# Performance work log

Measured on AMD Instinct MI355X. Metric: run time of the kernel, lower is better.

The kernel has to match this reference:

```python
import jax, jax.numpy as jnp
import numpy as np

N_NODES = 50000
N_EDGES = 400000
NUM_FEATS = 128
LATENT_DIM_Y = 64
HIDDEN = 512
OUT = 2


def gcn_conv(x, edge_index, W, b, num_nodes):
    """PyG GCNConv: add self-loops, symmetric normalization, x @ W then scatter-add."""
    x = x @ W  # [N, out_ch]
    loop = jnp.arange(num_nodes)
    row = jnp.concatenate([edge_index[0], loop])  # source nodes
    col = jnp.concatenate([edge_index[1], loop])  # target nodes
    deg = jax.ops.segment_sum(jnp.ones_like(col, dtype=x.dtype), col, num_segments=num_nodes)
    dinv = jnp.where(deg > 0, jax.lax.rsqrt(deg), 0.0)
    norm = dinv[row] * dinv[col]  # [E+N]
    msgs = norm[:, None] * x[row]  # gather source features, scale
    out = jax.ops.segment_sum(msgs, col, num_segments=num_nodes)
    return out + b


def setup_inputs() -> dict:
    key = jax.random.key(0)
    k1, k2, k3, k4, k5, k6, k7 = jax.random.split(key, 7)
    in_ch = NUM_FEATS + LATENT_DIM_Y
    inputs = {
        "edge_index": jax.random.randint(k1, (2, N_EDGES), 0, N_NODES),
        "X": jax.random.normal(k2, (N_NODES, NUM_FEATS), dtype=jnp.float32),
        "u_Y": jax.random.normal(k3, (N_NODES, LATENT_DIM_Y), dtype=jnp.float32),
        "W1": jax.random.normal(k4, (in_ch, HIDDEN), dtype=jnp.float32) / np.sqrt(in_ch),
        "b1": jnp.zeros((HIDDEN,), dtype=jnp.float32),
        "W2": jax.random.normal(k5, (HIDDEN, OUT), dtype=jnp.float32) / np.sqrt(HIDDEN),
        "b2": jnp.zeros((OUT,), dtype=jnp.float32),
    }
    return inputs


def reference(edge_index, X, u_Y, W1, b1, W2, b2):
    latent = jnp.concatenate([u_Y, X], axis=1)  # [N, latent+feats]
    h = jax.nn.relu(gcn_conv(latent, edge_index, W1, b1, N_NODES))
    y = gcn_conv(h, edge_index, W2, b2, N_NODES)
    # nn.Softmax() on a 2D tensor defaults to dim=1
    return jax.nn.softmax(y, axis=1)
```

## Files before the change

kernel.cpp:

```cpp
#include <hip/hip_runtime.h>

#define N_NODES 50000
#define N_EDGES 400000
#define FEATS   128
#define LAT     64
#define IN_CH   192
#define HID     512
#define MB      64
#define CAP     32

#define E4       100000
#define SC_BLKS  391
#define CVT_BLKS 4688
#define W1_BLKS  384

typedef __attribute__((ext_vector_type(8))) short bf16x8;
typedef __attribute__((ext_vector_type(4))) float f32x4;

static inline int cdiv(int a, int b) { return (a + b - 1) / b; }

__device__ __forceinline__ unsigned short f2bf(float f) {
    unsigned int u = __float_as_uint(f);
    u = (u + 0x7fffu + ((u >> 16) & 1u)) >> 16;
    return (unsigned short)u;
}
__device__ __forceinline__ unsigned int pack2bf(float lo, float hi) {
    return (unsigned int)f2bf(lo) | ((unsigned int)f2bf(hi) << 16);
}
__device__ __forceinline__ float bf_lo(unsigned int u) {
    return __uint_as_float(u << 16);
}
__device__ __forceinline__ float bf_hi(unsigned int u) {
    return __uint_as_float(u & 0xffff0000u);
}

__global__ __launch_bounds__(256) void
k_front(const int* __restrict__ ei, int* __restrict__ cursor, int* __restrict__ csr_src,
        const float* __restrict__ uY, const float* __restrict__ X,
        unsigned short* __restrict__ latent,
        const float* __restrict__ W1, unsigned short* __restrict__ W1f) {
    int bid = blockIdx.x;
    if (bid < SC_BLKS) {
        int i4 = bid * 256 + threadIdx.x;
        if (i4 < E4) {
            int4 r = ((const int4*)ei)[i4];
            int4 c = ((const int4*)(ei + N_EDGES))[i4];
            int p0 = atomicAdd(&cursor[c.x], 1);
            int p1 = atomicAdd(&cursor[c.y], 1);
            int p2 = atomicAdd(&cursor[c.z], 1);
            int p3 = atomicAdd(&cursor[c.w], 1);
            csr_src[c.x * CAP + p0] = r.x;
            csr_src[c.y * CAP + p1] = r.y;
            csr_src[c.z * CAP + p2] = r.z;
            csr_src[c.w * CAP + p3] = r.w;
        }
    } else if (bid < SC_BLKS + CVT_BLKS) {
        int idx = (bid - SC_BLKS) * 256 + threadIdx.x;
        if (idx < N_NODES * 24) {
            int i = idx / 24, q = idx % 24;
            const float4* uY4 = (const float4*)uY;
            const float4* X4  = (const float4*)X;
            float4 v0, v1;
            if (q < 8) {
                v0 = uY4[i * 16 + 2 * q];
                v1 = uY4[i * 16 + 2 * q + 1];
            } else {
                v0 = X4[i * 32 + 2 * (q - 8)];
                v1 = X4[i * 32 + 2 * (q - 8) + 1];
            }
            uint4 o;
            o.x = pack2bf(v0.x, v0.y);
            o.y = pack2bf(v0.z, v0.w);
            o.z = pack2bf(v1.x, v1.y);
            o.w = pack2bf(v1.z, v1.w);
            ((uint4*)latent)[idx] = o;
        }
    } else {
        int idx = (bid - SC_BLKS - CVT_BLKS) * 256 + threadIdx.x;
        if (idx < IN_CH * HID) {
            int k = idx / HID, n = idx % HID;
            int ntile = n >> 4, nn = n & 15;
            int kc = k >> 5, q = (k >> 3) & 3, j = k & 7;
            int dst = (((ntile * 6 + kc) * 64 + q * 16 + nn) << 3) + j;
            W1f[dst] = f2bf(W1[idx]);
        }
    }
}

__device__ __forceinline__ void fma6(float* acc, float wt,
                                     unsigned int A, unsigned int B, unsigned int C) {
    acc[0] = fmaf(wt, bf_lo(A), acc[0]);
    acc[1] = fmaf(wt, bf_hi(A), acc[1]);
    acc[2] = fmaf(wt, bf_lo(B), acc[2]);
    acc[3] = fmaf(wt, bf_hi(B), acc[3]);
    acc[4] = fmaf(wt, bf_lo(C), acc[4]);
    acc[5] = fmaf(wt, bf_hi(C), acc[5]);
}

__global__ __launch_bounds__(256) void
k_gather_agg(const int* __restrict__ cursor, const int* __restrict__ csr_src,
             const unsigned short* __restrict__ latent, unsigned short* __restrict__ agg) {
    int tid = threadIdx.x;
    int w   = blockIdx.x * 8 + (tid >> 5);
    int il  = tid & 31;
    if (w >= N_NODES) return;
    int lbase = tid & 32;
    const char* __restrict__ Lb = (const char*)latent;

    int deg = cursor[w];
    int raw = csr_src[w * CAP + max(il - 1, 0)];
    int rl  = (il == 0) ? w : min(max(raw, 0), N_NODES - 1);
    int dl  = cursor[rl];
    float di = rsqrtf((float)(deg + 1));
    float wl = (il == 0) ? di * di
             : ((il - 1 < deg) ? di * rsqrtf((float)(dl + 1)) : 0.f);
    int off_l = rl * 384;

    int R = (deg + 4) & ~3;

    float acc[6];
#pragma unroll
    for (int i = 0; i < 6; ++i) acc[i] = 0.f;

    auto LD = [&](int t, float& wt, uint2& U, unsigned int& C) {
        wt = __shfl(wl, lbase + t);
        int off = __shfl(off_l, lbase + t);
        const char* p = Lb + off;
        U = *(const uint2*)(p + 8 * il);
        C = *(const unsigned int*)(p + 256 + 4 * il);
    };

    float w0, w1, w2, w3; uint2 U0, U1, U2, U3; unsigned int C0, C1, C2, C3;
    LD(0, w0, U0, C0); LD(1, w1, U1, C1); LD(2, w2, U2, C2); LD(3, w3, U3, C3);
    int t = 0;
    for (; t + 7 < R; t += 4) {
        float v0, v1, v2, v3; uint2 V0, V1, V2, V3; unsigned int D0, D1, D2, D3;
        LD(t + 4, v0, V0, D0); LD(t + 5, v1, V1, D1);
        LD(t + 6, v2, V2, D2); LD(t + 7, v3, V3, D3);
        fma6(acc, w0, U0.x, U0.y, C0); fma6(acc, w1, U1.x, U1.y, C1);
        fma6(acc, w2, U2.x, U2.y, C2); fma6(acc, w3, U3.x, U3.y, C3);
        w0 = v0; U0 = V0; C0 = D0;  w1 = v1; U1 = V1; C1 = D1;
        w2 = v2; U2 = V2; C2 = D2;  w3 = v3; U3 = V3; C3 = D3;
    }
    fma6(acc, w0, U0.x, U0.y, C0); fma6(acc, w1, U1.x, U1.y, C1);
    fma6(acc, w2, U2.x, U2.y, C2); fma6(acc, w3, U3.x, U3.y, C3);

    unsigned int* op = (unsigned int*)agg + (size_t)w * 96;
    uint2 o;
    o.x = pack2bf(acc[0], acc[1]);
    o.y = pack2bf(acc[2], acc[3]);
    *((uint2*)op + il) = o;
    op[64 + il] = pack2bf(acc[4], acc[5]);
}

__global__ __launch_bounds__(256, 2) void
k_gemm_mfma(const unsigned short* __restrict__ agg, const unsigned short* __restrict__ W1f,
            const float* __restrict__ b1, const float* __restrict__ W2,
            float* __restrict__ y_pre) {
    __shared__ unsigned short Af[MB * IN_CH];
    __shared__ float red[4][MB][2];

    int t  = threadIdx.x;
    int m0 = blockIdx.x * MB;

    {
        const uint4* src = (const uint4*)agg;
        for (int idx = t; idx < MB * 24; idx += 256) {
            int row = idx / 24, c = idx % 24;
            int g = m0 + row;
            uint4 v = make_uint4(0u, 0u, 0u, 0u);
            if (g < N_NODES) v = src[(size_t)g * 24 + c];
            int mt = row >> 4, m = row & 15, kc = c >> 2, q = c & 3;
            ((uint4*)Af)[(mt * 6 + kc) * 64 + q * 16 + m] = v;
        }
    }
    __syncthreads();

    int wid = t >> 6, lane = t & 63;
    int nl = lane & 15, q = lane >> 4;

    float b1v[8], w2a[8], w2b[8];
#pragma unroll
    for (int nt = 0; nt < 8; ++nt) {
        int n = wid * 128 + nt * 16 + nl;
        b1v[nt] = b1[n];
        w2a[nt] = W2[n * 2 + 0];
        w2b[nt] = W2[n * 2 + 1];
    }

    f32x4 acc[4][8];
#pragma unroll
    for (int mt = 0; mt < 4; ++mt)
#pragma unroll
        for (int nt = 0; nt < 8; ++nt) acc[mt][nt] = (f32x4){0.f, 0.f, 0.f, 0.f};

    const bf16x8* Afv = (const bf16x8*)Af;
    const bf16x8* Bv  = (const bf16x8*)W1f;
#pragma unroll
    for (int kc = 0; kc < 6; ++kc) {
        bf16x8 a[4];
#pragma unroll
        for (int mt = 0; mt < 4; ++mt) a[mt] = Afv[(mt * 6 + kc) * 64 + lane];
#pragma unroll
        for (int nt = 0; nt < 8; ++nt) {
            bf16x8 b = Bv[((wid * 8 + nt) * 6 + kc) * 64 + lane];
#pragma unroll
            for (int mt = 0; mt < 4; ++mt)
                acc[mt][nt] = __builtin_amdgcn_mfma_f32_16x16x32_bf16(a[mt], b, acc[mt][nt], 0, 0, 0);
        }
    }

#pragma unroll
    for (int mt = 0; mt < 4; ++mt) {
#pragma unroll
        for (int r = 0; r < 4; ++r) {
            float p0 = 0.f, p1 = 0.f;
#pragma unroll
            for (int nt = 0; nt < 8; ++nt) {
                float h = fmaxf(acc[mt][nt][r] + b1v[nt], 0.f);
                p0 = fmaf(h, w2a[nt], p0);
                p1 = fmaf(h, w2b[nt], p1);
            }
#pragma unroll
            for (int off = 1; off < 16; off <<= 1) {
                p0 += __shfl_xor(p0, off);
                p1 += __shfl_xor(p1, off);
            }
            if (nl == 0) {
                int row = mt * 16 + q * 4 + r;
                red[wid][row][0] = p0;
                red[wid][row][1] = p1;
            }
        }
    }
    __syncthreads();
    if (t < MB * 2) {
        int row = t >> 1, j = t & 1;
        float s = red[0][row][j] + red[1][row][j] + red[2][row][j] + red[3][row][j];
        int g = m0 + row;
        if (g < N_NODES) y_pre[g * 2 + j] = s;
    }
}

__global__ __launch_bounds__(256) void
k_gather_y(const int* __restrict__ cursor, const int* __restrict__ csr_src,
           const float* __restrict__ y_pre, const float* __restrict__ b2,
           float* __restrict__ out) {
    int i  = blockIdx.x * 32 + (threadIdx.x >> 3);
    int l8 = threadIdx.x & 7;
    if (i >= N_NODES) return;
    const float2* __restrict__ yp = (const float2*)y_pre;

    int jlo = i * CAP;
    int deg  = cursor[i];
    int rawe = csr_src[jlo + max(l8 - 1, 0)];
    int raw2 = csr_src[jlo + l8 + 7];
    int raw1 = (l8 == 0) ? i : rawe;
    int r1 = min(max(raw1, 0), N_NODES - 1);
    int r2 = min(max(raw2, 0), N_NODES - 1);
    int d1 = cursor[r1], d2 = cursor[r2];
    float2 v1 = yp[r1];

    float di = rsqrtf((float)(deg + 1));
    float w1 = (l8 == 0) ? di
             : ((l8 - 1 < deg) ? rsqrtf((float)(d1 + 1)) : 0.f);
    float a0 = w1 * v1.x, a1 = w1 * v1.y;
    if (deg > 7) {
        float2 v2 = yp[r2];
        float w2 = (l8 + 7 < deg) ? rsqrtf((float)(d2 + 1)) : 0.f;
        a0 = fmaf(w2, v2.x, a0);
        a1 = fmaf(w2, v2.y, a1);
        for (int e = 15 + l8; e < deg; e += 8) {
            int r = csr_src[jlo + e];
            float wt = rsqrtf((float)(cursor[r] + 1));
            float2 v = yp[r];
            a0 = fmaf(wt, v.x, a0);
            a1 = fmaf(wt, v.y, a1);
        }
    }
#pragma unroll
    for (int off = 1; off < 8; off <<= 1) {
        a0 += __shfl_xor(a0, off);
        a1 += __shfl_xor(a1, off);
    }
    if (l8 == 0) {
        float ya = di * a0 + b2[0];
        float yb = di * a1 + b2[1];
        float mx = fmaxf(ya, yb);
        float e0 = expf(ya - mx);
        float e1 = expf(yb - mx);
        float inv = 1.0f / (e0 + e1);
        out[i * 2 + 0] = e0 * inv;
        out[i * 2 + 1] = e1 * inv;
    }
}


extern "C" void kernel_launch(void* const* d_in, const int* in_sizes, int n_in,
                              void* d_out, int out_size, void* d_ws, size_t ws_size,
                              hipStream_t stream) {
    const int*   ei = (const int*)d_in[0];
    const float* X  = (const float*)d_in[1];
    const float* uY = (const float*)d_in[2];
    const float* W1 = (const float*)d_in[3];
    const float* b1 = (const float*)d_in[4];
    const float* W2 = (const float*)d_in[5];
    const float* b2 = (const float*)d_in[6];
    float* out = (float*)d_out;

    char* ws = (char*)d_ws;
    auto carve = [&](size_t bytes) {
        char* p = ws;
        ws += (bytes + 255) & ~size_t(255);
        return p;
    };
    int*   cursor    = (int*)carve(N_NODES * sizeof(int));
    int*   csr_src   = (int*)carve((size_t)N_NODES * CAP * sizeof(int));
    unsigned short* latent = (unsigned short*)carve((size_t)N_NODES * IN_CH * 2);
    unsigned short* aggb   = (unsigned short*)carve((size_t)N_NODES * IN_CH * 2);
    unsigned short* W1f    = (unsigned short*)carve((size_t)IN_CH * HID * 2);
    float* y_pre     = (float*)carve((size_t)N_NODES * 2 * sizeof(float));

    hipMemsetAsync(cursor, 0, N_NODES * sizeof(int), stream);

    k_front     <<<SC_BLKS + CVT_BLKS + W1_BLKS, 256, 0, stream>>>(
                      ei, cursor, csr_src, uY, X, latent, W1, W1f);

    k_gather_agg<<<cdiv(N_NODES, 8), 256, 0, stream>>>(
                      cursor, csr_src, latent, aggb);

    k_gemm_mfma <<<cdiv(N_NODES, MB), 256, 0, stream>>>(aggb, W1f, b1, W2, y_pre);

    k_gather_y  <<<cdiv(N_NODES, 32), 256, 0, stream>>>(
                      cursor, csr_src, y_pre, b2, out);
}
```

Baseline: 171.8 us.

## Fuse fp32-to-bf16 latent conversion into gather; read fp32 inputs directly

Drops the separate pass that concatenated uY and X into a bf16 latent buffer. The gather-aggregate kernel now reads fp32 rows straight from uY and X for each neighbor. The prefetch depth in the gather loop is also doubled from 4 to 8 neighbors. This saves writing and re-reading a 19 MB intermediate, but each random neighbor gather now pulls twice as many bytes (768 B instead of 384 B per row) and needs more registers.

```diff
diff --git a/kernel.cpp b/kernel.cpp
--- a/kernel.cpp
+++ b/kernel.cpp
@@ -11,7 +11,6 @@
 
 #define E4       100000
 #define SC_BLKS  391
-#define CVT_BLKS 4688
 #define W1_BLKS  384
 
 typedef __attribute__((ext_vector_type(8))) short bf16x8;
@@ -27,17 +26,9 @@
 __device__ __forceinline__ unsigned int pack2bf(float lo, float hi) {
     return (unsigned int)f2bf(lo) | ((unsigned int)f2bf(hi) << 16);
 }
-__device__ __forceinline__ float bf_lo(unsigned int u) {
-    return __uint_as_float(u << 16);
-}
-__device__ __forceinline__ float bf_hi(unsigned int u) {
-    return __uint_as_float(u & 0xffff0000u);
-}
 
 __global__ __launch_bounds__(256) void
 k_front(const int* __restrict__ ei, int* __restrict__ cursor, int* __restrict__ csr_src,
-        const float* __restrict__ uY, const float* __restrict__ X,
-        unsigned short* __restrict__ latent,
         const float* __restrict__ W1, unsigned short* __restrict__ W1f) {
     int bid = blockIdx.x;
     if (bid < SC_BLKS) {
@@ -54,29 +45,8 @@
             csr_src[c.z * CAP + p2] = r.z;
             csr_src[c.w * CAP + p3] = r.w;
         }
-    } else if (bid < SC_BLKS + CVT_BLKS) {
+    } else {
         int idx = (bid - SC_BLKS) * 256 + threadIdx.x;
-        if (idx < N_NODES * 24) {
-            int i = idx / 24, q = idx % 24;
-            const float4* uY4 = (const float4*)uY;
-            const float4* X4  = (const float4*)X;
-            float4 v0, v1;
-            if (q < 8) {
-                v0 = uY4[i * 16 + 2 * q];
-                v1 = uY4[i * 16 + 2 * q + 1];
-            } else {
-                v0 = X4[i * 32 + 2 * (q - 8)];
-                v1 = X4[i * 32 + 2 * (q - 8) + 1];
-            }
-            uint4 o;
-            o.x = pack2bf(v0.x, v0.y);
-            o.y = pack2bf(v0.z, v0.w);
-            o.z = pack2bf(v1.x, v1.y);
-            o.w = pack2bf(v1.z, v1.w);
-            ((uint4*)latent)[idx] = o;
-        }
-    } else {
-        int idx = (bid - SC_BLKS - CVT_BLKS) * 256 + threadIdx.x;
         if (idx < IN_CH * HID) {
             int k = idx / HID, n = idx % HID;
             int ntile = n >> 4, nn = n & 15;
@@ -87,25 +57,24 @@
     }
 }
 
-__device__ __forceinline__ void fma6(float* acc, float wt,
-                                     unsigned int A, unsigned int B, unsigned int C) {
-    acc[0] = fmaf(wt, bf_lo(A), acc[0]);
-    acc[1] = fmaf(wt, bf_hi(A), acc[1]);
-    acc[2] = fmaf(wt, bf_lo(B), acc[2]);
-    acc[3] = fmaf(wt, bf_hi(B), acc[3]);
-    acc[4] = fmaf(wt, bf_lo(C), acc[4]);
-    acc[5] = fmaf(wt, bf_hi(C), acc[5]);
+__device__ __forceinline__ void fma6(float* acc, float wt, float4 F, float2 G) {
+    acc[0] = fmaf(wt, F.x, acc[0]);
+    acc[1] = fmaf(wt, F.y, acc[1]);
+    acc[2] = fmaf(wt, F.z, acc[2]);
+    acc[3] = fmaf(wt, F.w, acc[3]);
+    acc[4] = fmaf(wt, G.x, acc[4]);
+    acc[5] = fmaf(wt, G.y, acc[5]);
 }
 
 __global__ __launch_bounds__(256) void
 k_gather_agg(const int* __restrict__ cursor, const int* __restrict__ csr_src,
-             const unsigned short* __restrict__ latent, unsigned short* __restrict__ agg) {
+             const float* __restrict__ uY, const float* __restrict__ X,
+             unsigned short* __restrict__ agg) {
     int tid = threadIdx.x;
     int w   = blockIdx.x * 8 + (tid >> 5);
     int il  = tid & 31;
     if (w >= N_NODES) return;
     int lbase = tid & 32;
-    const char* __restrict__ Lb = (const char*)latent;
 
     int deg = cursor[w];
     int raw = csr_src[w * CAP + max(il - 1, 0)];
@@ -114,36 +83,50 @@
     float di = rsqrtf((float)(deg + 1));
     float wl = (il == 0) ? di * di
              : ((il - 1 < deg) ? di * rsqrtf((float)(dl + 1)) : 0.f);
-    int off_l = rl * 384;
-
-    int R = (deg + 4) & ~3;
+
+    int R = (deg + 8) & ~7;
 
     float acc[6];
 #pragma unroll
     for (int i = 0; i < 6; ++i) acc[i] = 0.f;
 
-    auto LD = [&](int t, float& wt, uint2& U, unsigned int& C) {
+    auto LD = [&](int t, float& wt, float4& F, float2& G) {
         wt = __shfl(wl, lbase + t);
-        int off = __shfl(off_l, lbase + t);
-        const char* p = Lb + off;
-        U = *(const uint2*)(p + 8 * il);
-        C = *(const unsigned int*)(p + 256 + 4 * il);
+        int r = __shfl(rl, lbase + t);
+        const float* px = X + (size_t)r * FEATS;
+        const float4* p4 = (il < 16) ? (const float4*)(uY + (size_t)r * LAT) + il
+                                     : (const float4*)px + (il - 16);
+        F = *p4;
+        G = ((const float2*)px)[32 + il];
     };
 
-    float w0, w1, w2, w3; uint2 U0, U1, U2, U3; unsigned int C0, C1, C2, C3;
-    LD(0, w0, U0, C0); LD(1, w1, U1, C1); LD(2, w2, U2, C2); LD(3, w3, U3, C3);
+    float w0, w1, w2, w3, w4, w5, w6, w7;
+    float4 F0, F1, F2, F3, F4, F5, F6, F7;
+    float2 G0, G1, G2, G3, G4, G5, G6, G7;
+    LD(0, w0, F0, G0); LD(1, w1, F1, G1); LD(2, w2, F2, G2); LD(3, w3, F3, G3);
+    LD(4, w4, F4, G4); LD(5, w5, F5, G5); LD(6, w6, F6, G6); LD(7, w7, F7, G7);
     int t = 0;
-    for (; t + 7 < R; t += 4) {
-        float v0, v1, v2, v3; uint2 V0, V1, V2, V3; unsigned int D0, D1, D2, D3;
-        LD(t + 4, v0, V0, D0); LD(t + 5, v1, V1, D1);
-        LD(t + 6, v2, V2, D2); LD(t + 7, v3, V3, D3);
-        fma6(acc, w0, U0.x, U0.y, C0); fma6(acc, w1, U1.x, U1.y, C1);
-        fma6(acc, w2, U2.x, U2.y, C2); fma6(acc, w3, U3.x, U3.y, C3);
-        w0 = v0; U0 = V0; C0 = D0;  w1 = v1; U1 = V1; C1 = D1;
-        w2 = v2; U2 = V2; C2 = D2;  w3 = v3; U3 = V3; C3 = D3;
-    }
-    fma6(acc, w0, U0.x, U0.y, C0); fma6(acc, w1, U1.x, U1.y, C1);
-    fma6(acc, w2, U2.x, U2.y, C2); fma6(acc, w3, U3.x, U3.y, C3);
+    for (; t + 15 < R; t += 8) {
+        float v0, v1, v2, v3, v4, v5, v6, v7;
+        float4 A0, A1, A2, A3, A4, A5, A6, A7;
+        float2 B0, B1, B2, B3, B4, B5, B6, B7;
+        LD(t + 8,  v0, A0, B0); LD(t + 9,  v1, A1, B1);
+        LD(t + 10, v2, A2, B2); LD(t + 11, v3, A3, B3);
+        LD(t + 12, v4, A4, B4); LD(t + 13, v5, A5, B5);
+        LD(t + 14, v6, A6, B6); LD(t + 15, v7, A7, B7);
+        fma6(acc, w0, F0, G0); fma6(acc, w1, F1, G1);
+        fma6(acc, w2, F2, G2); fma6(acc, w3, F3, G3);
+        fma6(acc, w4, F4, G4); fma6(acc, w5, F5, G5);
+        fma6(acc, w6, F6, G6); fma6(acc, w7, F7, G7);
+        w0 = v0; F0 = A0; G0 = B0;  w1 = v1; F1 = A1; G1 = B1;
+        w2 = v2; F2 = A2; G2 = B2;  w3 = v3; F3 = A3; G3 = B3;
+        w4 = v4; F4 = A4; G4 = B4;  w5 = v5; F5 = A5; G5 = B5;
+        w6 = v6; F6 = A6; G6 = B6;  w7 = v7; F7 = A7; G7 = B7;
+    }
+    fma6(acc, w0, F0, G0); fma6(acc, w1, F1, G1);
+    fma6(acc, w2, F2, G2); fma6(acc, w3, F3, G3);
+    fma6(acc, w4, F4, G4); fma6(acc, w5, F5, G5);
+    fma6(acc, w6, F6, G6); fma6(acc, w7, F7, G7);
 
     unsigned int* op = (unsigned int*)agg + (size_t)w * 96;
     uint2 o;
@@ -316,18 +299,17 @@
     };
     int*   cursor    = (int*)carve(N_NODES * sizeof(int));
     int*   csr_src   = (int*)carve((size_t)N_NODES * CAP * sizeof(int));
-    unsigned short* latent = (unsigned short*)carve((size_t)N_NODES * IN_CH * 2);
-    unsigned short* aggb   = (unsigned short*)carve((size_t)N_NODES * IN_CH * 2);
-    unsigned short* W1f    = (unsigned short*)carve((size_t)IN_CH * HID * 2);
+    unsigned short* aggb = (unsigned short*)carve((size_t)N_NODES * IN_CH * 2);
+    unsigned short* W1f  = (unsigned short*)carve((size_t)IN_CH * HID * 2);
     float* y_pre     = (float*)carve((size_t)N_NODES * 2 * sizeof(float));
 
     hipMemsetAsync(cursor, 0, N_NODES * sizeof(int), stream);
 
-    k_front     <<<SC_BLKS + CVT_BLKS + W1_BLKS, 256, 0, stream>>>(
-                      ei, cursor, csr_src, uY, X, latent, W1, W1f);
+    k_front     <<<SC_BLKS + W1_BLKS, 256, 0, stream>>>(
+                      ei, cursor, csr_src, W1, W1f);
 
     k_gather_agg<<<cdiv(N_NODES, 8), 256, 0, stream>>>(
-                      cursor, csr_src, latent, aggb);
+                      cursor, csr_src, uY, X, aggb);
 
     k_gemm_mfma <<<cdiv(N_NODES, MB), 256, 0, stream>>>(aggb, W1f, b1, W2, y_pre);
 
```

Result: slower. 188.3 us (+9.6%).
